# Optimization experiments

Measured on AMD Instinct MI355X. Metric: run time of the kernel, lower is better.

Reference implementation:

```python
import jax, jax.numpy as jnp
import numpy as np

B, A, D, NHEAD, DFF = 8, 128, 256, 8, 2048
EPS = 1e-5


def _ln(x, g, b):
    m = x.mean(-1, keepdims=True)
    v = ((x - m) ** 2).mean(-1, keepdims=True)
    return (x - m) * jax.lax.rsqrt(v + EPS) * g + b


def setup_inputs() -> dict:
    key = jax.random.key(0)
    ks = jax.random.split(key, 32)

    def lin_w(k, i, o):
        s = 1.0 / np.sqrt(i)
        return jax.random.uniform(k, (i, o), jnp.float32, -s, s)

    def lin_b(k, i, o):
        s = 1.0 / np.sqrt(i)
        return jax.random.uniform(k, (o,), jnp.float32, -s, s)

    inp = {
        "src": jax.random.normal(ks[0], (B, A, D), jnp.float32),
        "self_pos_embed": jax.random.normal(ks[1], (B, A, D), jnp.float32),
        "relative_pose_embed": jax.random.normal(ks[2], (B, A, A, D), jnp.float32),
        # q/k/v content projections (D -> D)
        "Wq": lin_w(ks[3], D, D), "bq": lin_b(ks[4], D, D),
        "Wk": lin_w(ks[5], D, D), "bk": lin_b(ks[6], D, D),
        "Wv": lin_w(ks[7], D, D), "bv": lin_b(ks[8], D, D),
        # positional projections (D -> D)
        "Wqp": lin_w(ks[9], D, D), "bqp": lin_b(ks[10], D, D),
        "Wkp": lin_w(ks[11], D, D), "bkp": lin_b(ks[12], D, D),
        "Wvp": lin_w(ks[13], D, D), "bvp": lin_b(ks[14], D, D),
        # FFN
        "W1": lin_w(ks[15], D, DFF), "b1": lin_b(ks[16], D, DFF),
        "W2": lin_w(ks[17], DFF, D), "b2": lin_b(ks[18], DFF, D),
        # LayerNorms
        "g1": jnp.ones((D,), jnp.float32), "be1": jnp.zeros((D,), jnp.float32),
        "g2": jnp.ones((D,), jnp.float32), "be2": jnp.zeros((D,), jnp.float32),
    }
    return inp


def reference(src, self_pos_embed, relative_pose_embed,
              Wq, bq, Wk, bk, Wv, bv, Wqp, bqp, Wkp, bkp, Wvp, bvp,
              W1, b1, W2, b2, g1, be1, g2, be2):
    b_, a_, d_ = src.shape
    H = NHEAD
    hd = (2 * d_) // H          # head dim of concat(q, q_pos) embedding
    H2 = H // 2                  # heads covering the content half / pos half
    vhd = d_ // H                # value head dim (vdim = d_model)
    scale = 1.0 / np.sqrt(hd)

    # Projections. Note: v = sa_v_proj(sa_k_proj(src)) per the original code.
    q_pos = self_pos_embed @ Wqp + bqp                    # (B,A,D)
    k_pos = relative_pose_embed @ Wkp + bkp               # (B,A,A,D)
    v_pos = relative_pose_embed @ Wvp + bvp               # (B,A,A,D)
    k_base = src @ Wk + bk                                # (B,A,D) (broadcast over q instead of repeat)
    v_base = k_base @ Wv + bv                             # (B,A,D)
    q = src @ Wq + bq                                     # (B,A,D)

    # concat([q, q_pos]) / concat([k, k_pos]) split into per-head pieces:
    # first H2 heads come from the content half, last H2 from the pos half.
    qc = q.reshape(b_, a_, H2, hd)
    qp = q_pos.reshape(b_, a_, H2, hd)
    kc = k_base.reshape(b_, a_, H2, hd)
    kp = k_pos.reshape(b_, a_, a_, H2, hd)

    sc = jnp.einsum('bqhe,bkhe->bhqk', qc, kc)            # content heads (k broadcast over q)
    sp = jnp.einsum('bqhe,bqkhe->bhqk', qp, kp)           # relative-pos heads
    scores = jnp.concatenate([sc, sp], axis=1) * scale    # (B,H,A,A)
    attn = jax.nn.softmax(scores, axis=-1)

    vb = v_base.reshape(b_, a_, H, vhd)
    vp = (v_pos).reshape(b_, a_, a_, H, vhd)
    out = jnp.einsum('bhqk,bkhe->bqhe', attn, vb) + \
          jnp.einsum('bhqk,bqkhe->bqhe', attn, vp)        # (B,A,H,vhd)
    src2 = out.reshape(b_, a_, d_)

    x = _ln(src + src2, g1, be1)
    ff = jax.nn.relu(x @ W1 + b1) @ W2 + b2
    return _ln(x + ff, g2, be2)
```

## Files before the change

kernel.cpp:

```cpp
#include <hip/hip_runtime.h>
#include <hip/hip_bf16.h>
#include <math.h>

#define kB 8
#define kA 128
#define kD 256
#define kF 2048
#define NROW 1024

typedef __attribute__((ext_vector_type(8))) __bf16 bf16x8;
typedef __attribute__((ext_vector_type(4))) __bf16 bf16x4;
typedef __attribute__((ext_vector_type(4))) float f32x4;

#define MFMA16(a, b, c) __builtin_amdgcn_mfma_f32_16x16x32_bf16(a, b, c, 0, 0, 0)

__device__ __forceinline__ bf16x8 frag_f32(const float* p) {
    float4 a = *(const float4*)p;
    float4 b = *(const float4*)(p + 4);
    bf16x8 v;
    v[0] = (__bf16)a.x; v[1] = (__bf16)a.y; v[2] = (__bf16)a.z; v[3] = (__bf16)a.w;
    v[4] = (__bf16)b.x; v[5] = (__bf16)b.y; v[6] = (__bf16)b.z; v[7] = (__bf16)b.w;
    return v;
}
__device__ __forceinline__ bf16x8 frag_bf16(const __bf16* p) {
    return *(const bf16x8*)p;
}

__global__ __launch_bounds__(256) void prep_transpose_kernel(
    const float* __restrict__ Wq, const float* __restrict__ Wk,
    const float* __restrict__ Wqp, const float* __restrict__ Wv,
    const float* __restrict__ Wvp, const float* __restrict__ W1,
    const float* __restrict__ W2,
    __bf16* WqT, __bf16* WkT, __bf16* WqpT, __bf16* WvT, __bf16* WvpT,
    __bf16* W1T, __bf16* W2T)
{
    int bid = blockIdx.x;
    const float* in; __bf16* out; int R, C;
    if (bid < 80) {
        int m = bid >> 4; bid &= 15;
        const float* ins[5] = {Wq, Wk, Wqp, Wv, Wvp};
        __bf16* outs[5] = {WqT, WkT, WqpT, WvT, WvpT};
        in = ins[m]; out = outs[m]; R = 256; C = 256;
    } else if (bid < 208) { bid -= 80; in = W1; out = W1T; R = 256; C = 2048; }
    else { bid -= 208; in = W2; out = W2T; R = 2048; C = 256; }
    int tilesC = C >> 6;
    int r0 = (bid / tilesC) << 6, c0 = (bid % tilesC) << 6;
    __shared__ float tile[64][65];
    int t = threadIdx.x, tr = t >> 6, tc = t & 63;
#pragma unroll
    for (int i = 0; i < 16; ++i)
        tile[tr + i * 4][tc] = in[(size_t)(r0 + tr + i * 4) * C + c0 + tc];
    __syncthreads();
#pragma unroll
    for (int i = 0; i < 16; ++i) {
        int oc = tr + i * 4;
        out[(size_t)(c0 + oc) * R + r0 + tc] = (__bf16)tile[tc][oc];
    }
}

__global__ __launch_bounds__(256) void proj3_mfma(
    const float* __restrict__ src, const float* __restrict__ spe,
    const __bf16* __restrict__ WqT, const __bf16* __restrict__ WkT,
    const __bf16* __restrict__ WqpT,
    const float* __restrict__ bq, const float* __restrict__ bk,
    const float* __restrict__ bqp,
    float* __restrict__ q, float* __restrict__ kb, float* __restrict__ qpos)
{
    const float* X; const __bf16* WT; const float* bias; float* Y;
    if (blockIdx.z == 0)      { X = src; WT = WqT;  bias = bq;  Y = q; }
    else if (blockIdx.z == 1) { X = src; WT = WkT;  bias = bk;  Y = kb; }
    else                      { X = spe; WT = WqpT; bias = bqp; Y = qpos; }
    int t = threadIdx.x, w = t >> 6, l = t & 63;
    int p = l & 15, g = l >> 4;
    int m0 = blockIdx.x * 64 + w * 16;
    int n0 = blockIdx.y * 64;
    f32x4 acc[4] = {{0.f,0.f,0.f,0.f},{0.f,0.f,0.f,0.f},{0.f,0.f,0.f,0.f},{0.f,0.f,0.f,0.f}};
#pragma unroll
    for (int ks = 0; ks < 8; ++ks) {
        bf16x8 a = frag_f32(X + (size_t)(m0 + p) * 256 + ks * 32 + g * 8);
#pragma unroll
        for (int nt = 0; nt < 4; ++nt) {
            bf16x8 bb = frag_bf16(WT + (size_t)(n0 + nt * 16 + p) * 256 + ks * 32 + g * 8);
            acc[nt] = MFMA16(a, bb, acc[nt]);
        }
    }
#pragma unroll
    for (int nt = 0; nt < 4; ++nt) {
        int col = n0 + nt * 16 + p;
        float bv = bias[col];
#pragma unroll
        for (int i = 0; i < 4; ++i)
            Y[(size_t)(m0 + g * 4 + i) * 256 + col] = acc[nt][i] + bv;
    }
}

__global__ __launch_bounds__(256) void projv_mfma(
    const float* __restrict__ kb, const __bf16* __restrict__ WvT,
    const float* __restrict__ bv, __bf16* __restrict__ vbT)
{
    int t = threadIdx.x, w = t >> 6, l = t & 63;
    int p = l & 15, g = l >> 4;
    int m0 = blockIdx.x * 64 + w * 16;
    int n0 = blockIdx.y * 64;
    f32x4 acc[4] = {{0.f,0.f,0.f,0.f},{0.f,0.f,0.f,0.f},{0.f,0.f,0.f,0.f},{0.f,0.f,0.f,0.f}};
#pragma unroll
    for (int ks = 0; ks < 8; ++ks) {
        bf16x8 a = frag_f32(kb + (size_t)(m0 + p) * 256 + ks * 32 + g * 8);
#pragma unroll
        for (int nt = 0; nt < 4; ++nt) {
            bf16x8 bb = frag_bf16(WvT + (size_t)(n0 + nt * 16 + p) * 256 + ks * 32 + g * 8);
            acc[nt] = MFMA16(a, bb, acc[nt]);
        }
    }
#pragma unroll
    for (int nt = 0; nt < 4; ++nt) {
        int e = n0 + nt * 16 + p;
        float bvv = bv[e];
#pragma unroll
        for (int i = 0; i < 4; ++i) {
            int row = m0 + g * 4 + i;
            vbT[((size_t)(row >> 7) * 256 + e) * 128 + (row & 127)] =
                (__bf16)(acc[nt][i] + bvv);
        }
    }
}

__global__ __launch_bounds__(256) void u_mfma(
    const float* __restrict__ qpos, const float* __restrict__ Wkp,
    __bf16* __restrict__ u_buf)
{
    int t = threadIdx.x, w = t >> 6, l = t & 63;
    int p = l & 15, g = l >> 4;
    int m0 = blockIdx.x * 16;
    int h = blockIdx.y;
    f32x4 acc[4] = {{0.f,0.f,0.f,0.f},{0.f,0.f,0.f,0.f},{0.f,0.f,0.f,0.f},{0.f,0.f,0.f,0.f}};
#pragma unroll
    for (int ks = 0; ks < 2; ++ks) {
        bf16x8 a = frag_f32(qpos + (size_t)(m0 + p) * 256 + h * 64 + ks * 32 + g * 8);
#pragma unroll
        for (int nt = 0; nt < 4; ++nt) {
            int c0 = w * 64 + nt * 16;
            bf16x8 bb = frag_f32(Wkp + (size_t)(c0 + p) * 256 + h * 64 + ks * 32 + g * 8);
            acc[nt] = MFMA16(a, bb, acc[nt]);
        }
    }
#pragma unroll
    for (int nt = 0; nt < 4; ++nt) {
        int c = w * 64 + nt * 16 + p;
#pragma unroll
        for (int i = 0; i < 4; ++i)
            u_buf[((size_t)(m0 + g * 4 + i) * 4 + h) * 256 + c] = (__bf16)acc[nt][i];
    }
}

__global__ __launch_bounds__(256) void con_mfma(
    const float* __restrict__ q, const float* __restrict__ kb,
    float* __restrict__ s_con)
{
    int t = threadIdx.x, w = t >> 6, l = t & 63;
    int p = l & 15, g = l >> 4;
    int b = blockIdx.x, h = blockIdx.y;
    f32x4 acc[2][8];
#pragma unroll
    for (int mm = 0; mm < 2; ++mm)
#pragma unroll
        for (int nt = 0; nt < 8; ++nt) acc[mm][nt] = (f32x4){0.f,0.f,0.f,0.f};
#pragma unroll
    for (int ks = 0; ks < 2; ++ks) {
        bf16x8 a0 = frag_f32(q + (size_t)(b * 128 + w * 32 + p) * 256 + h * 64 + ks * 32 + g * 8);
        bf16x8 a1 = frag_f32(q + (size_t)(b * 128 + w * 32 + 16 + p) * 256 + h * 64 + ks * 32 + g * 8);
#pragma unroll
        for (int nt = 0; nt < 8; ++nt) {
            bf16x8 bb = frag_f32(kb + (size_t)(b * 128 + nt * 16 + p) * 256 + h * 64 + ks * 32 + g * 8);
            acc[0][nt] = MFMA16(a0, bb, acc[0][nt]);
            acc[1][nt] = MFMA16(a1, bb, acc[1][nt]);
        }
    }
    float* out = s_con + (size_t)(b * 4 + h) * 16384;
#pragma unroll
    for (int mm = 0; mm < 2; ++mm)
#pragma unroll
        for (int nt = 0; nt < 8; ++nt)
#pragma unroll
            for (int i = 0; i < 4; ++i)
                out[(size_t)(w * 32 + mm * 16 + g * 4 + i) * 128 + nt * 16 + p] = acc[mm][nt][i];
}

__global__ __launch_bounds__(256, 2) void attn_mfma(
    const float* __restrict__ src, const float* __restrict__ rel,
    const __bf16* __restrict__ u_buf, const float* __restrict__ s_con,
    const __bf16* __restrict__ vbT, const __bf16* __restrict__ WvpT,
    const float* __restrict__ qpos, const float* __restrict__ bkp,
    const float* __restrict__ bvp, const float* __restrict__ g1,
    const float* __restrict__ be1, float* __restrict__ x_out)
{
    const int t = threadIdx.x, w = t >> 6, l = t & 63;
    const int p = l & 15, g = l >> 4;
    const int qi = blockIdx.x, b = blockIdx.y;
    const int row = b * 128 + qi;

    __shared__ __bf16 Gt[256 * 128];
    __shared__ __bf16 A_lds[16 * 136];
    __shared__ float s_lds[128][9];
    __shared__ float out_lds[256];
    __shared__ float beta_lds[4];
    __shared__ float redA[4], redB[4];

    {
        float v = qpos[(size_t)row * 256 + w * 64 + l] * bkp[w * 64 + l];
#pragma unroll
        for (int sh = 32; sh; sh >>= 1) v += __shfl_xor(v, sh, 64);
        if (l == 0) beta_lds[w] = v;
    }

    {
        f32x4 sacc[2] = {{0.f,0.f,0.f,0.f},{0.f,0.f,0.f,0.f}};
        f32x4 gacc[2][16];
#pragma unroll
        for (int mt = 0; mt < 2; ++mt)
#pragma unroll
            for (int nt = 0; nt < 16; ++nt) gacc[mt][nt] = (f32x4){0.f,0.f,0.f,0.f};
        const float* Rbase = rel + (size_t)row * 128 * 256;
        for (int cs = 0; cs < 8; ++cs) {
            int c0 = cs * 32;
            bf16x8 ua = frag_bf16(u_buf + ((size_t)row * 4 + (p & 3)) * 256 + c0 + g * 8);
            bf16x8 r0 = frag_f32(Rbase + (size_t)(w * 32 + p) * 256 + c0 + g * 8);
            bf16x8 r1 = frag_f32(Rbase + (size_t)(w * 32 + 16 + p) * 256 + c0 + g * 8);
            sacc[0] = MFMA16(ua, r0, sacc[0]);
            sacc[1] = MFMA16(ua, r1, sacc[1]);
#pragma unroll
            for (int nt = 0; nt < 16; ++nt) {
                bf16x8 wv = frag_bf16(WvpT + (size_t)(nt * 16 + p) * 256 + c0 + g * 8);
                gacc[0][nt] = MFMA16(r0, wv, gacc[0][nt]);
                gacc[1][nt] = MFMA16(r1, wv, gacc[1][nt]);
            }
        }
        if (g == 0) {
#pragma unroll
            for (int mt = 0; mt < 2; ++mt)
#pragma unroll
                for (int i = 0; i < 4; ++i)
                    s_lds[w * 32 + mt * 16 + p][4 + i] = sacc[mt][i];
        }
#pragma unroll
        for (int mt = 0; mt < 2; ++mt) {
            int kbase = w * 32 + mt * 16 + g * 4;
            int kb8 = kbase >> 3, klo = kbase & 7;
#pragma unroll
            for (int nt = 0; nt < 16; ++nt) {
                int e = nt * 16 + p;
                bf16x4 v;
                v[0] = (__bf16)gacc[mt][nt][0]; v[1] = (__bf16)gacc[mt][nt][1];
                v[2] = (__bf16)gacc[mt][nt][2]; v[3] = (__bf16)gacc[mt][nt][3];
                *(bf16x4*)&Gt[e * 128 + ((kb8 ^ (e & 7)) << 3) + klo] = v;
            }
        }
    }
    {
        const float* sc = s_con + (size_t)(b * 4) * 16384 + qi * 128;
#pragma unroll
        for (int i = 0; i < 2; ++i) {
            int idx = t + i * 256;
            int h = idx >> 7, k = idx & 127;
            s_lds[k][h] = sc[(size_t)h * 16384 + k];
        }
    }
    __syncthreads();

    {
        int h = t >> 5, l32 = t & 31;
        float beta = (h >= 4) ? beta_lds[h - 4] : 0.f;
        float v0 = (s_lds[l32][h] + beta) * 0.125f;
        float v1 = (s_lds[l32 + 32][h] + beta) * 0.125f;
        float v2 = (s_lds[l32 + 64][h] + beta) * 0.125f;
        float v3 = (s_lds[l32 + 96][h] + beta) * 0.125f;
        float m = fmaxf(fmaxf(v0, v1), fmaxf(v2, v3));
#pragma unroll
        for (int sh = 16; sh; sh >>= 1) m = fmaxf(m, __shfl_xor(m, sh, 64));
        v0 = __expf(v0 - m); v1 = __expf(v1 - m);
        v2 = __expf(v2 - m); v3 = __expf(v3 - m);
        float s = v0 + v1 + v2 + v3;
#pragma unroll
        for (int sh = 16; sh; sh >>= 1) s += __shfl_xor(s, sh, 64);
        float inv = 1.0f / s;
        A_lds[h * 136 + l32]      = (__bf16)(v0 * inv);
        A_lds[h * 136 + l32 + 32] = (__bf16)(v1 * inv);
        A_lds[h * 136 + l32 + 64] = (__bf16)(v2 * inv);
        A_lds[h * 136 + l32 + 96] = (__bf16)(v3 * inv);
    }
    __syncthreads();

    {
        f32x4 oacc[4] = {{0.f,0.f,0.f,0.f},{0.f,0.f,0.f,0.f},{0.f,0.f,0.f,0.f},{0.f,0.f,0.f,0.f}};
        const __bf16* vbase = vbT + (size_t)b * 256 * 128;
#pragma unroll
        for (int ks = 0; ks < 4; ++ks) {
            bf16x8 af = frag_bf16(A_lds + p * 136 + ks * 32 + g * 8);
#pragma unroll
            for (int nt = 0; nt < 4; ++nt) {
                int e = w * 64 + nt * 16 + p;
                bf16x8 vf = frag_bf16(vbase + (size_t)e * 128 + ks * 32 + g * 8);
                oacc[nt] = MFMA16(af, vf, oacc[nt]);
                bf16x8 gf = frag_bf16(&Gt[e * 128 + (((ks * 4 + g) ^ (e & 7)) << 3)]);
                oacc[nt] = MFMA16(af, gf, oacc[nt]);
            }
        }
#pragma unroll
        for (int nt = 0; nt < 4; ++nt) {
            int h = w * 2 + (nt >> 1);
            if (g == (h >> 2)) {
                int i = h & 3;
                float v = (i == 0) ? oacc[nt][0] : (i == 1) ? oacc[nt][1]
                        : (i == 2) ? oacc[nt][2] : oacc[nt][3];
                out_lds[w * 64 + nt * 16 + p] = v;
            }
        }
    }
    __syncthreads();

    {
        float y = src[(size_t)row * 256 + t] + out_lds[t] + bvp[t];
        float s1 = y, s2 = y * y;
#pragma unroll
        for (int sh = 32; sh; sh >>= 1) {
            s1 += __shfl_xor(s1, sh, 64);
            s2 += __shfl_xor(s2, sh, 64);
        }
        if (l == 0) { redA[w] = s1; redB[w] = s2; }
        __syncthreads();
        s1 = redA[0] + redA[1] + redA[2] + redA[3];
        s2 = redB[0] + redB[1] + redB[2] + redB[3];
        float mean = s1 * (1.0f / 256.0f);
        float var = fmaxf(s2 * (1.0f / 256.0f) - mean * mean, 0.0f);
        float inv = rsqrtf(var + 1e-5f);
        x_out[(size_t)row * 256 + t] = (y - mean) * inv * g1[t] + be1[t];
    }
}

__global__ __launch_bounds__(256) void ffn_mfma(
    const float* __restrict__ x, const __bf16* __restrict__ W1T,
    const float* __restrict__ b1, const __bf16* __restrict__ W2T,
    float* __restrict__ part)
{
    __shared__ __bf16 h_lds[32 * 264];
    int t = threadIdx.x, w = t >> 6, l = t & 63;
    int p = l & 15, g = l >> 4;
    int m0 = blockIdx.x * 32;
    int c0 = blockIdx.y * 256;
    int mt = w & 1, nh = w >> 1;

    {
        f32x4 acc[8];
#pragma unroll
        for (int nt = 0; nt < 8; ++nt) acc[nt] = (f32x4){0.f,0.f,0.f,0.f};
#pragma unroll
        for (int ks = 0; ks < 8; ++ks) {
            bf16x8 a = frag_f32(x + (size_t)(m0 + mt * 16 + p) * 256 + ks * 32 + g * 8);
#pragma unroll
            for (int nt = 0; nt < 8; ++nt) {
                bf16x8 bb = frag_bf16(W1T + (size_t)(c0 + nh * 128 + nt * 16 + p) * 256 + ks * 32 + g * 8);
                acc[nt] = MFMA16(a, bb, acc[nt]);
            }
        }
#pragma unroll
        for (int nt = 0; nt < 8; ++nt) {
            int col = nh * 128 + nt * 16 + p;
            float bv = b1[c0 + col];
#pragma unroll
            for (int i = 0; i < 4; ++i)
                h_lds[(mt * 16 + g * 4 + i) * 264 + col] =
                    (__bf16)fmaxf(acc[nt][i] + bv, 0.f);
        }
    }
    __syncthreads();
    {
        f32x4 acc[8];
#pragma unroll
        for (int nt = 0; nt < 8; ++nt) acc[nt] = (f32x4){0.f,0.f,0.f,0.f};
#pragma unroll
        for (int ks = 0; ks < 8; ++ks) {
            bf16x8 a = frag_bf16(h_lds + (mt * 16 + p) * 264 + ks * 32 + g * 8);
#pragma unroll
            for (int nt = 0; nt < 8; ++nt) {
                bf16x8 bb = frag_bf16(W2T + (size_t)(nh * 128 + nt * 16 + p) * 2048 + c0 + ks * 32 + g * 8);
                acc[nt] = MFMA16(a, bb, acc[nt]);
            }
        }
#pragma unroll
        for (int nt = 0; nt < 8; ++nt) {
            int e = nh * 128 + nt * 16 + p;
#pragma unroll
            for (int i = 0; i < 4; ++i)
                part[((size_t)blockIdx.y * NROW + m0 + mt * 16 + g * 4 + i) * 256 + e] = acc[nt][i];
        }
    }
}

__global__ __launch_bounds__(256) void ffn_ln2_kernel(
    const float* __restrict__ x, const float* __restrict__ part,
    const float* __restrict__ b2, const float* __restrict__ g2,
    const float* __restrict__ be2, float* __restrict__ out)
{
    __shared__ float red1[4][4], red2[4][4];
    const int t = threadIdx.x;
    const int r0 = blockIdx.x * 4;
    const int wv = t >> 6, lane = t & 63;
    float b2v = b2[t];
    float yv[4];
#pragma unroll
    for (int r = 0; r < 4; ++r) {
        size_t idx = (size_t)(r0 + r) * 256 + t;
        float y = x[idx] + b2v;
#pragma unroll
        for (int c = 0; c < 8; ++c) y += part[idx + (size_t)c * (NROW * 256)];
        yv[r] = y;
        float s1 = y, s2 = y * y;
#pragma unroll
        for (int sh = 32; sh; sh >>= 1) {
            s1 += __shfl_xor(s1, sh, 64);
            s2 += __shfl_xor(s2, sh, 64);
        }
        if (lane == 0) { red1[r][wv] = s1; red2[r][wv] = s2; }
    }
    __syncthreads();
    float g = g2[t], be = be2[t];
#pragma unroll
    for (int r = 0; r < 4; ++r) {
        float s1 = red1[r][0] + red1[r][1] + red1[r][2] + red1[r][3];
        float s2 = red2[r][0] + red2[r][1] + red2[r][2] + red2[r][3];
        float mean = s1 * (1.0f / 256.0f);
        float var = fmaxf(s2 * (1.0f / 256.0f) - mean * mean, 0.0f);
        float inv = rsqrtf(var + 1e-5f);
        out[(size_t)(r0 + r) * 256 + t] = (yv[r] - mean) * inv * g + be;
    }
}

extern "C" void kernel_launch(void* const* d_in, const int* in_sizes, int n_in,
                              void* d_out, int out_size, void* d_ws, size_t ws_size,
                              hipStream_t stream)
{
    const float* src  = (const float*)d_in[0];
    const float* spe  = (const float*)d_in[1];
    const float* rel  = (const float*)d_in[2];
    const float* Wq   = (const float*)d_in[3];
    const float* bq   = (const float*)d_in[4];
    const float* Wk   = (const float*)d_in[5];
    const float* bk   = (const float*)d_in[6];
    const float* Wv   = (const float*)d_in[7];
    const float* bv   = (const float*)d_in[8];
    const float* Wqp  = (const float*)d_in[9];
    const float* bqp  = (const float*)d_in[10];
    const float* Wkp  = (const float*)d_in[11];
    const float* bkp  = (const float*)d_in[12];
    const float* Wvp  = (const float*)d_in[13];
    const float* bvp  = (const float*)d_in[14];
    const float* W1   = (const float*)d_in[15];
    const float* b1   = (const float*)d_in[16];
    const float* W2   = (const float*)d_in[17];
    const float* b2   = (const float*)d_in[18];
    const float* g1   = (const float*)d_in[19];
    const float* be1  = (const float*)d_in[20];
    const float* g2   = (const float*)d_in[21];
    const float* be2  = (const float*)d_in[22];

    char* wsb = (char*)d_ws;
    const size_t MB = 1 << 20;
    float*  xbuf  = (float*)(wsb);
    float*  q     = (float*)(wsb + 1 * MB);
    float*  kbuf  = (float*)(wsb + 2 * MB);
    float*  qpos  = (float*)(wsb + 3 * MB);
    __bf16* u_buf = (__bf16*)(wsb + 4 * MB);
    float*  s_con = (float*)(wsb + 6 * MB);
    __bf16* vbT   = (__bf16*)(wsb + 8 * MB);
    __bf16* WqT   = (__bf16*)(wsb + 8 * MB + 512 * 1024);
    __bf16* WkT   = WqT + 65536;
    __bf16* WqpT  = WkT + 65536;
    __bf16* WvT   = WqpT + 65536;
    __bf16* WvpT  = WvT + 65536;
    __bf16* W1T   = (__bf16*)(wsb + 9 * MB + 128 * 1024);
    __bf16* W2T   = (__bf16*)(wsb + 10 * MB + 128 * 1024);
    float*  part  = (float*)(wsb + 1 * MB);

    prep_transpose_kernel<<<336, 256, 0, stream>>>(Wq, Wk, Wqp, Wv, Wvp, W1, W2,
                                                   WqT, WkT, WqpT, WvT, WvpT, W1T, W2T);
    proj3_mfma<<<dim3(16, 4, 3), 256, 0, stream>>>(src, spe, WqT, WkT, WqpT,
                                                   bq, bk, bqp, q, kbuf, qpos);
    projv_mfma<<<dim3(16, 4), 256, 0, stream>>>(kbuf, WvT, bv, vbT);
    u_mfma<<<dim3(64, 4), 256, 0, stream>>>(qpos, Wkp, u_buf);
    con_mfma<<<dim3(8, 4), 256, 0, stream>>>(q, kbuf, s_con);
    attn_mfma<<<dim3(kA, kB), 256, 0, stream>>>(src, rel, u_buf, s_con, vbT, WvpT,
                                                qpos, bkp, bvp, g1, be1, xbuf);
    ffn_mfma<<<dim3(32, 8), 256, 0, stream>>>(xbuf, W1T, b1, W2T, part);
    ffn_ln2_kernel<<<256, 256, 0, stream>>>(xbuf, part, b2, g2, be2, (float*)d_out);
}
```

Before: 351.9 us.

## Reassociate relative-pos attention: apply attention to rel rows first, then project with Wvp

```diff
diff --git a/kernel.cpp b/kernel.cpp
--- a/kernel.cpp
+++ b/kernel.cpp
@@ -9,7 +9,6 @@
 #define NROW 1024
 
 typedef __attribute__((ext_vector_type(8))) __bf16 bf16x8;
-typedef __attribute__((ext_vector_type(4))) __bf16 bf16x4;
 typedef __attribute__((ext_vector_type(4))) float f32x4;
 
 #define MFMA16(a, b, c) __builtin_amdgcn_mfma_f32_16x16x32_bf16(a, b, c, 0, 0, 0)
@@ -26,23 +25,22 @@
     return *(const bf16x8*)p;
 }
 
-__global__ __launch_bounds__(256) void prep_transpose_kernel(
+__global__ __launch_bounds__(256) void prep1_kernel(
     const float* __restrict__ Wq, const float* __restrict__ Wk,
-    const float* __restrict__ Wqp, const float* __restrict__ Wv,
-    const float* __restrict__ Wvp, const float* __restrict__ W1,
-    const float* __restrict__ W2,
-    __bf16* WqT, __bf16* WkT, __bf16* WqpT, __bf16* WvT, __bf16* WvpT,
+    const float* __restrict__ Wv, const float* __restrict__ Wvp,
+    const float* __restrict__ W1, const float* __restrict__ W2,
+    __bf16* WqT, __bf16* WkT, __bf16* WvT, __bf16* WvpT,
     __bf16* W1T, __bf16* W2T)
 {
     int bid = blockIdx.x;
     const float* in; __bf16* out; int R, C;
-    if (bid < 80) {
+    if (bid < 64) {
         int m = bid >> 4; bid &= 15;
-        const float* ins[5] = {Wq, Wk, Wqp, Wv, Wvp};
-        __bf16* outs[5] = {WqT, WkT, WqpT, WvT, WvpT};
+        const float* ins[4] = {Wq, Wk, Wv, Wvp};
+        __bf16* outs[4] = {WqT, WkT, WvT, WvpT};
         in = ins[m]; out = outs[m]; R = 256; C = 256;
-    } else if (bid < 208) { bid -= 80; in = W1; out = W1T; R = 256; C = 2048; }
-    else { bid -= 208; in = W2; out = W2T; R = 2048; C = 256; }
+    } else if (bid < 192) { bid -= 64; in = W1; out = W1T; R = 256; C = 2048; }
+    else { bid -= 192; in = W2; out = W2T; R = 2048; C = 256; }
     int tilesC = C >> 6;
     int r0 = (bid / tilesC) << 6, c0 = (bid % tilesC) << 6;
     __shared__ float tile[64][65];
@@ -58,26 +56,64 @@
     }
 }
 
-__global__ __launch_bounds__(256) void proj3_mfma(
-    const float* __restrict__ src, const float* __restrict__ spe,
+__global__ __launch_bounds__(256) void prep2_kernel(
+    const float* __restrict__ Wqp, const float* __restrict__ Wkp,
+    const float* __restrict__ bqp, __bf16* __restrict__ M_hT,
+    float* __restrict__ ubias)
+{
+    int bid = blockIdx.x;
+    int t = threadIdx.x;
+    if (bid < 16) {
+        int h = bid >> 2, cb = bid & 3;
+        int w = t >> 6, l = t & 63, p = l & 15, g = l >> 4;
+        int m0 = cb * 64 + w * 16;
+        f32x4 acc[16];
+#pragma unroll
+        for (int nt = 0; nt < 16; ++nt) acc[nt] = (f32x4){0.f, 0.f, 0.f, 0.f};
+#pragma unroll
+        for (int ks = 0; ks < 2; ++ks) {
+            bf16x8 a = frag_f32(Wkp + (size_t)(m0 + p) * 256 + h * 64 + ks * 32 + g * 8);
+#pragma unroll
+            for (int nt = 0; nt < 16; ++nt) {
+                bf16x8 bb = frag_f32(Wqp + (size_t)(nt * 16 + p) * 256 + h * 64 + ks * 32 + g * 8);
+                acc[nt] = MFMA16(a, bb, acc[nt]);
+            }
+        }
+#pragma unroll
+        for (int nt = 0; nt < 16; ++nt)
+#pragma unroll
+            for (int i = 0; i < 4; ++i)
+                M_hT[((size_t)h * 256 + m0 + g * 4 + i) * 256 + nt * 16 + p] = (__bf16)acc[nt][i];
+    } else {
+        int c = t;
+#pragma unroll
+        for (int h = 0; h < 4; ++h) {
+            float s = 0.f;
+            for (int e = 0; e < 64; ++e) s += bqp[h * 64 + e] * Wkp[(size_t)c * 256 + h * 64 + e];
+            ubias[h * 256 + c] = s;
+        }
+    }
+}
+
+__global__ __launch_bounds__(256) void proj_kernel(
+    const float* __restrict__ src,
     const __bf16* __restrict__ WqT, const __bf16* __restrict__ WkT,
-    const __bf16* __restrict__ WqpT,
     const float* __restrict__ bq, const float* __restrict__ bk,
-    const float* __restrict__ bqp,
-    float* __restrict__ q, float* __restrict__ kb, float* __restrict__ qpos)
-{
-    const float* X; const __bf16* WT; const float* bias; float* Y;
-    if (blockIdx.z == 0)      { X = src; WT = WqT;  bias = bq;  Y = q; }
-    else if (blockIdx.z == 1) { X = src; WT = WkT;  bias = bk;  Y = kb; }
-    else                      { X = spe; WT = WqpT; bias = bqp; Y = qpos; }
+    float* __restrict__ q, float* __restrict__ kb)
+{
+    const __bf16* WT; const float* bias; float* Y;
+    if (blockIdx.z == 0) { WT = WqT; bias = bq; Y = q; }
+    else                 { WT = WkT; bias = bk; Y = kb; }
     int t = threadIdx.x, w = t >> 6, l = t & 63;
     int p = l & 15, g = l >> 4;
     int m0 = blockIdx.x * 64 + w * 16;
     int n0 = blockIdx.y * 64;
-    f32x4 acc[4] = {{0.f,0.f,0.f,0.f},{0.f,0.f,0.f,0.f},{0.f,0.f,0.f,0.f},{0.f,0.f,0.f,0.f}};
+    f32x4 acc[4];
+#pragma unroll
+    for (int nt = 0; nt < 4; ++nt) acc[nt] = (f32x4){0.f, 0.f, 0.f, 0.f};
 #pragma unroll
     for (int ks = 0; ks < 8; ++ks) {
-        bf16x8 a = frag_f32(X + (size_t)(m0 + p) * 256 + ks * 32 + g * 8);
+        bf16x8 a = frag_f32(src + (size_t)(m0 + p) * 256 + ks * 32 + g * 8);
 #pragma unroll
         for (int nt = 0; nt < 4; ++nt) {
             bf16x8 bb = frag_bf16(WT + (size_t)(n0 + nt * 16 + p) * 256 + ks * 32 + g * 8);
@@ -94,7 +130,7 @@
     }
 }
 
-__global__ __launch_bounds__(256) void projv_mfma(
+__global__ __launch_bounds__(256) void projv_kernel(
     const float* __restrict__ kb, const __bf16* __restrict__ WvT,
     const float* __restrict__ bv, __bf16* __restrict__ vbT)
 {
@@ -102,7 +138,9 @@
     int p = l & 15, g = l >> 4;
     int m0 = blockIdx.x * 64 + w * 16;
     int n0 = blockIdx.y * 64;
-    f32x4 acc[4] = {{0.f,0.f,0.f,0.f},{0.f,0.f,0.f,0.f},{0.f,0.f,0.f,0.f},{0.f,0.f,0.f,0.f}};
+    f32x4 acc[4];
+#pragma unroll
+    for (int nt = 0; nt < 4; ++nt) acc[nt] = (f32x4){0.f, 0.f, 0.f, 0.f};
 #pragma unroll
     for (int ks = 0; ks < 8; ++ks) {
         bf16x8 a = frag_f32(kb + (size_t)(m0 + p) * 256 + ks * 32 + g * 8);
@@ -119,280 +157,259 @@
 #pragma unroll
         for (int i = 0; i < 4; ++i) {
             int row = m0 + g * 4 + i;
-            vbT[((size_t)(row >> 7) * 256 + e) * 128 + (row & 127)] =
-                (__bf16)(acc[nt][i] + bvv);
-        }
-    }
-}
-
-__global__ __launch_bounds__(256) void u_mfma(
-    const float* __restrict__ qpos, const float* __restrict__ Wkp,
-    __bf16* __restrict__ u_buf)
+            vbT[((size_t)(row >> 7) * 256 + e) * 128 + (row & 127)] = (__bf16)(acc[nt][i] + bvv);
+        }
+    }
+}
+
+__global__ __launch_bounds__(256) void u_kernel(
+    const float* __restrict__ spe, const __bf16* __restrict__ M_hT,
+    const float* __restrict__ ubias, __bf16* __restrict__ u_buf)
 {
     int t = threadIdx.x, w = t >> 6, l = t & 63;
     int p = l & 15, g = l >> 4;
-    int m0 = blockIdx.x * 16;
     int h = blockIdx.y;
-    f32x4 acc[4] = {{0.f,0.f,0.f,0.f},{0.f,0.f,0.f,0.f},{0.f,0.f,0.f,0.f},{0.f,0.f,0.f,0.f}};
-#pragma unroll
-    for (int ks = 0; ks < 2; ++ks) {
-        bf16x8 a = frag_f32(qpos + (size_t)(m0 + p) * 256 + h * 64 + ks * 32 + g * 8);
-#pragma unroll
-        for (int nt = 0; nt < 4; ++nt) {
-            int c0 = w * 64 + nt * 16;
-            bf16x8 bb = frag_f32(Wkp + (size_t)(c0 + p) * 256 + h * 64 + ks * 32 + g * 8);
+    int m0 = blockIdx.x * 64 + w * 16;
+    f32x4 acc[16];
+#pragma unroll
+    for (int nt = 0; nt < 16; ++nt) acc[nt] = (f32x4){0.f, 0.f, 0.f, 0.f};
+#pragma unroll
+    for (int ks = 0; ks < 8; ++ks) {
+        bf16x8 a = frag_f32(spe + (size_t)(m0 + p) * 256 + ks * 32 + g * 8);
+#pragma unroll
+        for (int nt = 0; nt < 16; ++nt) {
+            bf16x8 bb = frag_bf16(M_hT + ((size_t)h * 256 + nt * 16 + p) * 256 + ks * 32 + g * 8);
             acc[nt] = MFMA16(a, bb, acc[nt]);
         }
     }
 #pragma unroll
-    for (int nt = 0; nt < 4; ++nt) {
-        int c = w * 64 + nt * 16 + p;
+    for (int nt = 0; nt < 16; ++nt) {
+        float ub = ubias[h * 256 + nt * 16 + p];
 #pragma unroll
         for (int i = 0; i < 4; ++i)
-            u_buf[((size_t)(m0 + g * 4 + i) * 4 + h) * 256 + c] = (__bf16)acc[nt][i];
-    }
-}
-
-__global__ __launch_bounds__(256) void con_mfma(
-    const float* __restrict__ q, const float* __restrict__ kb,
-    float* __restrict__ s_con)
-{
-    int t = threadIdx.x, w = t >> 6, l = t & 63;
-    int p = l & 15, g = l >> 4;
-    int b = blockIdx.x, h = blockIdx.y;
-    f32x4 acc[2][8];
-#pragma unroll
-    for (int mm = 0; mm < 2; ++mm)
-#pragma unroll
-        for (int nt = 0; nt < 8; ++nt) acc[mm][nt] = (f32x4){0.f,0.f,0.f,0.f};
-#pragma unroll
-    for (int ks = 0; ks < 2; ++ks) {
-        bf16x8 a0 = frag_f32(q + (size_t)(b * 128 + w * 32 + p) * 256 + h * 64 + ks * 32 + g * 8);
-        bf16x8 a1 = frag_f32(q + (size_t)(b * 128 + w * 32 + 16 + p) * 256 + h * 64 + ks * 32 + g * 8);
-#pragma unroll
-        for (int nt = 0; nt < 8; ++nt) {
-            bf16x8 bb = frag_f32(kb + (size_t)(b * 128 + nt * 16 + p) * 256 + h * 64 + ks * 32 + g * 8);
-            acc[0][nt] = MFMA16(a0, bb, acc[0][nt]);
-            acc[1][nt] = MFMA16(a1, bb, acc[1][nt]);
-        }
-    }
-    float* out = s_con + (size_t)(b * 4 + h) * 16384;
-#pragma unroll
-    for (int mm = 0; mm < 2; ++mm)
-#pragma unroll
-        for (int nt = 0; nt < 8; ++nt)
-#pragma unroll
-            for (int i = 0; i < 4; ++i)
-                out[(size_t)(w * 32 + mm * 16 + g * 4 + i) * 128 + nt * 16 + p] = acc[mm][nt][i];
-}
-
-__global__ __launch_bounds__(256, 2) void attn_mfma(
-    const float* __restrict__ src, const float* __restrict__ rel,
-    const __bf16* __restrict__ u_buf, const float* __restrict__ s_con,
-    const __bf16* __restrict__ vbT, const __bf16* __restrict__ WvpT,
-    const float* __restrict__ qpos, const float* __restrict__ bkp,
-    const float* __restrict__ bvp, const float* __restrict__ g1,
-    const float* __restrict__ be1, float* __restrict__ x_out)
+            u_buf[((size_t)(m0 + g * 4 + i) * 4 + h) * 256 + nt * 16 + p] = (__bf16)(acc[nt][i] + ub);
+    }
+}
+
+__global__ __launch_bounds__(512, 4) void attn1_kernel(
+    const float* __restrict__ rel, const float* __restrict__ q,
+    const float* __restrict__ kb, const __bf16* __restrict__ u_buf,
+    __bf16* __restrict__ A_all, __bf16* __restrict__ r_all)
 {
     const int t = threadIdx.x, w = t >> 6, l = t & 63;
     const int p = l & 15, g = l >> 4;
     const int qi = blockIdx.x, b = blockIdx.y;
     const int row = b * 128 + qi;
 
-    __shared__ __bf16 Gt[256 * 128];
+    __shared__ __bf16 RT[32768];
     __shared__ __bf16 A_lds[16 * 136];
     __shared__ float s_lds[128][9];
-    __shared__ float out_lds[256];
-    __shared__ float beta_lds[4];
-    __shared__ float redA[4], redB[4];
+
+    for (int i = t; i < 8 * 136; i += 512) A_lds[8 * 136 + i] = (__bf16)0.f;
 
     {
-        float v = qpos[(size_t)row * 256 + w * 64 + l] * bkp[w * 64 + l];
-#pragma unroll
-        for (int sh = 32; sh; sh >>= 1) v += __shfl_xor(v, sh, 64);
-        if (l == 0) beta_lds[w] = v;
-    }
+        const float* Rbase = rel + (size_t)row * 128 * 256;
+        const int k = w * 16 + p;
+        const int ko = k >> 3, klo = (k & 7) * 2;
+        f32x4 sacc = (f32x4){0.f, 0.f, 0.f, 0.f};
+#pragma unroll
+        for (int cs = 0; cs < 8; ++cs) {
+            int c0 = cs * 32 + g * 8;
+            bf16x8 rf = frag_f32(Rbase + (size_t)k * 256 + c0);
+            bf16x8 ua = frag_bf16(u_buf + ((size_t)row * 4 + (p & 3)) * 256 + c0);
+            sacc = MFMA16(ua, rf, sacc);
+#pragma unroll
+            for (int j = 0; j < 8; ++j) {
+                int byte = (c0 + j) * 256 + ((ko ^ j) << 4) + klo;
+                *(__bf16*)((char*)RT + byte) = rf[j];
+            }
+        }
+        f32x4 cacc[4];
+#pragma unroll
+        for (int h = 0; h < 4; ++h) cacc[h] = (f32x4){0.f, 0.f, 0.f, 0.f};
+#pragma unroll
+        for (int h = 0; h < 4; ++h)
+#pragma unroll
+            for (int ks = 0; ks < 2; ++ks) {
+                bf16x8 qa = frag_f32(q + (size_t)row * 256 + h * 64 + ks * 32 + g * 8);
+                bf16x8 kf = frag_f32(kb + ((size_t)b * 128 + k) * 256 + h * 64 + ks * 32 + g * 8);
+                cacc[h] = MFMA16(qa, kf, cacc[h]);
+            }
+        if (g == 0) {
+#pragma unroll
+            for (int i = 0; i < 4; ++i) s_lds[k][4 + i] = sacc[i];
+#pragma unroll
+            for (int h = 0; h < 4; ++h) s_lds[k][h] = cacc[h][0];
+        }
+    }
+    __syncthreads();
 
     {
-        f32x4 sacc[2] = {{0.f,0.f,0.f,0.f},{0.f,0.f,0.f,0.f}};
-        f32x4 gacc[2][16];
-#pragma unroll
-        for (int mt = 0; mt < 2; ++mt)
-#pragma unroll
-            for (int nt = 0; nt < 16; ++nt) gacc[mt][nt] = (f32x4){0.f,0.f,0.f,0.f};
-        const float* Rbase = rel + (size_t)row * 128 * 256;
+        float v0 = s_lds[l][w] * 0.125f;
+        float v1 = s_lds[l + 64][w] * 0.125f;
+        float m = fmaxf(v0, v1);
+#pragma unroll
+        for (int sh = 32; sh; sh >>= 1) m = fmaxf(m, __shfl_xor(m, sh, 64));
+        v0 = __expf(v0 - m); v1 = __expf(v1 - m);
+        float s = v0 + v1;
+#pragma unroll
+        for (int sh = 32; sh; sh >>= 1) s += __shfl_xor(s, sh, 64);
+        float inv = 1.0f / s;
+        __bf16 e0 = (__bf16)(v0 * inv), e1 = (__bf16)(v1 * inv);
+        A_lds[w * 136 + l] = e0;
+        A_lds[w * 136 + l + 64] = e1;
+        __bf16* Ag = A_all + ((size_t)(b * 8 + w) * 128 + qi) * 128;
+        Ag[l] = e0; Ag[l + 64] = e1;
+    }
+    __syncthreads();
+
+    {
+        f32x4 racc[2];
+        racc[0] = (f32x4){0.f, 0.f, 0.f, 0.f};
+        racc[1] = (f32x4){0.f, 0.f, 0.f, 0.f};
+#pragma unroll
+        for (int ks = 0; ks < 4; ++ks) {
+            bf16x8 af = *(const bf16x8*)&A_lds[p * 136 + ks * 32 + g * 8];
+#pragma unroll
+            for (int nt = 0; nt < 2; ++nt) {
+                int c = w * 32 + nt * 16 + p;
+                bf16x8 bfr = *(const bf16x8*)((char*)RT + c * 256 + (((ks * 4 + g) ^ (c & 7)) << 4));
+                racc[nt] = MFMA16(af, bfr, racc[nt]);
+            }
+        }
+        if (g < 2) {
+#pragma unroll
+            for (int nt = 0; nt < 2; ++nt)
+#pragma unroll
+                for (int i = 0; i < 4; ++i)
+                    r_all[((size_t)row * 8 + g * 4 + i) * 256 + w * 32 + nt * 16 + p] =
+                        (__bf16)racc[nt][i];
+        }
+    }
+}
+
+__global__ __launch_bounds__(256) void attn2_kernel(
+    const float* __restrict__ src, const __bf16* __restrict__ A_all,
+    const __bf16* __restrict__ r_all, const __bf16* __restrict__ vbT,
+    const __bf16* __restrict__ WvpT, const float* __restrict__ bvp,
+    const float* __restrict__ g1, const float* __restrict__ be1,
+    float* __restrict__ x_out)
+{
+    const int t = threadIdx.x, w = t >> 6, l = t & 63;
+    const int p = l & 15, g = l >> 4;
+    const int r0 = blockIdx.x * 4;
+    const int b = r0 >> 7, q0 = r0 & 127;
+    __shared__ float ymem[4][260];
+
+    f32x4 oacc[4];
+#pragma unroll
+    for (int nt = 0; nt < 4; ++nt) oacc[nt] = (f32x4){0.f, 0.f, 0.f, 0.f};
+#pragma unroll
+    for (int nt = 0; nt < 4; ++nt) {
+        int e0 = w * 64 + nt * 16;
+        int h = e0 >> 5;
+#pragma unroll
+        for (int ks = 0; ks < 4; ++ks) {
+            bf16x8 af = frag_bf16(A_all + ((size_t)(b * 8 + h) * 128 + q0 + p) * 128 + ks * 32 + g * 8);
+            bf16x8 vf = frag_bf16(vbT + ((size_t)b * 256 + e0 + p) * 128 + ks * 32 + g * 8);
+            oacc[nt] = MFMA16(af, vf, oacc[nt]);
+        }
+#pragma unroll
         for (int cs = 0; cs < 8; ++cs) {
-            int c0 = cs * 32;
-            bf16x8 ua = frag_bf16(u_buf + ((size_t)row * 4 + (p & 3)) * 256 + c0 + g * 8);
-            bf16x8 r0 = frag_f32(Rbase + (size_t)(w * 32 + p) * 256 + c0 + g * 8);
-            bf16x8 r1 = frag_f32(Rbase + (size_t)(w * 32 + 16 + p) * 256 + c0 + g * 8);
-            sacc[0] = MFMA16(ua, r0, sacc[0]);
-            sacc[1] = MFMA16(ua, r1, sacc[1]);
-#pragma unroll
-            for (int nt = 0; nt < 16; ++nt) {
-                bf16x8 wv = frag_bf16(WvpT + (size_t)(nt * 16 + p) * 256 + c0 + g * 8);
-                gacc[0][nt] = MFMA16(r0, wv, gacc[0][nt]);
-                gacc[1][nt] = MFMA16(r1, wv, gacc[1][nt]);
-            }
-        }
-        if (g == 0) {
-#pragma unroll
-            for (int mt = 0; mt < 2; ++mt)
-#pragma unroll
-                for (int i = 0; i < 4; ++i)
-                    s_lds[w * 32 + mt * 16 + p][4 + i] = sacc[mt][i];
-        }
-#pragma unroll
-        for (int mt = 0; mt < 2; ++mt) {
-            int kbase = w * 32 + mt * 16 + g * 4;
-            int kb8 = kbase >> 3, klo = kbase & 7;
-#pragma unroll
-            for (int nt = 0; nt < 16; ++nt) {
-                int e = nt * 16 + p;
-                bf16x4 v;
-                v[0] = (__bf16)gacc[mt][nt][0]; v[1] = (__bf16)gacc[mt][nt][1];
-                v[2] = (__bf16)gacc[mt][nt][2]; v[3] = (__bf16)gacc[mt][nt][3];
-                *(bf16x4*)&Gt[e * 128 + ((kb8 ^ (e & 7)) << 3) + klo] = v;
-            }
-        }
-    }
+            bf16x8 rf = frag_bf16(r_all + ((size_t)(r0 + p) * 8 + h) * 256 + cs * 32 + g * 8);
+            bf16x8 wf = frag_bf16(WvpT + (size_t)(e0 + p) * 256 + cs * 32 + g * 8);
+            oacc[nt] = MFMA16(rf, wf, oacc[nt]);
+        }
+    }
+    if (g == 0) {
+#pragma unroll
+        for (int nt = 0; nt < 4; ++nt)
+#pragma unroll
+            for (int i = 0; i < 4; ++i)
+                ymem[i][w * 64 + nt * 16 + p] = oacc[nt][i];
+    }
+    __syncthreads();
+
     {
-        const float* sc = s_con + (size_t)(b * 4) * 16384 + qi * 128;
-#pragma unroll
-        for (int i = 0; i < 2; ++i) {
-            int idx = t + i * 256;
-            int h = idx >> 7, k = idx & 127;
-            s_lds[k][h] = sc[(size_t)h * 16384 + k];
-        }
-    }
-    __syncthreads();
-
-    {
-        int h = t >> 5, l32 = t & 31;
-        float beta = (h >= 4) ? beta_lds[h - 4] : 0.f;
-        float v0 = (s_lds[l32][h] + beta) * 0.125f;
-        float v1 = (s_lds[l32 + 32][h] + beta) * 0.125f;
-        float v2 = (s_lds[l32 + 64][h] + beta) * 0.125f;
-        float v3 = (s_lds[l32 + 96][h] + beta) * 0.125f;
-        float m = fmaxf(fmaxf(v0, v1), fmaxf(v2, v3));
-#pragma unroll
-        for (int sh = 16; sh; sh >>= 1) m = fmaxf(m, __shfl_xor(m, sh, 64));
-        v0 = __expf(v0 - m); v1 = __expf(v1 - m);
-        v2 = __expf(v2 - m); v3 = __expf(v3 - m);
-        float s = v0 + v1 + v2 + v3;
-#pragma unroll
-        for (int sh = 16; sh; sh >>= 1) s += __shfl_xor(s, sh, 64);
-        float inv = 1.0f / s;
-        A_lds[h * 136 + l32]      = (__bf16)(v0 * inv);
-        A_lds[h * 136 + l32 + 32] = (__bf16)(v1 * inv);
-        A_lds[h * 136 + l32 + 64] = (__bf16)(v2 * inv);
-        A_lds[h * 136 + l32 + 96] = (__bf16)(v3 * inv);
-    }
-    __syncthreads();
-
-    {
-        f32x4 oacc[4] = {{0.f,0.f,0.f,0.f},{0.f,0.f,0.f,0.f},{0.f,0.f,0.f,0.f},{0.f,0.f,0.f,0.f}};
-        const __bf16* vbase = vbT + (size_t)b * 256 * 128;
-#pragma unroll
-        for (int ks = 0; ks < 4; ++ks) {
-            bf16x8 af = frag_bf16(A_lds + p * 136 + ks * 32 + g * 8);
-#pragma unroll
-            for (int nt = 0; nt < 4; ++nt) {
-                int e = w * 64 + nt * 16 + p;
-                bf16x8 vf = frag_bf16(vbase + (size_t)e * 128 + ks * 32 + g * 8);
-                oacc[nt] = MFMA16(af, vf, oacc[nt]);
-                bf16x8 gf = frag_bf16(&Gt[e * 128 + (((ks * 4 + g) ^ (e & 7)) << 3)]);
-                oacc[nt] = MFMA16(af, gf, oacc[nt]);
-            }
-        }
-#pragma unroll
-        for (int nt = 0; nt < 4; ++nt) {
-            int h = w * 2 + (nt >> 1);
-            if (g == (h >> 2)) {
-                int i = h & 3;
-                float v = (i == 0) ? oacc[nt][0] : (i == 1) ? oacc[nt][1]
-                        : (i == 2) ? oacc[nt][2] : oacc[nt][3];
-                out_lds[w * 64 + nt * 16 + p] = v;
-            }
-        }
-    }
-    __syncthreads();
-
-    {
-        float y = src[(size_t)row * 256 + t] + out_lds[t] + bvp[t];
-        float s1 = y, s2 = y * y;
+        float vals[4];
+        float s1 = 0.f, s2 = 0.f;
+#pragma unroll
+        for (int j = 0; j < 4; ++j) {
+            int e = l + j * 64;
+            float v = src[(size_t)(r0 + w) * 256 + e] + ymem[w][e] + bvp[e];
+            vals[j] = v; s1 += v; s2 += v * v;
+        }
 #pragma unroll
         for (int sh = 32; sh; sh >>= 1) {
             s1 += __shfl_xor(s1, sh, 64);
             s2 += __shfl_xor(s2, sh, 64);
         }
-        if (l == 0) { redA[w] = s1; redB[w] = s2; }
-        __syncthreads();
-        s1 = redA[0] + redA[1] + redA[2] + redA[3];
-        s2 = redB[0] + redB[1] + redB[2] + redB[3];
         float mean = s1 * (1.0f / 256.0f);
         float var = fmaxf(s2 * (1.0f / 256.0f) - mean * mean, 0.0f);
         float inv = rsqrtf(var + 1e-5f);
-        x_out[(size_t)row * 256 + t] = (y - mean) * inv * g1[t] + be1[t];
-    }
-}
-
-__global__ __launch_bounds__(256) void ffn_mfma(
+#pragma unroll
+        for (int j = 0; j < 4; ++j) {
+            int e = l + j * 64;
+            x_out[(size_t)(r0 + w) * 256 + e] = (vals[j] - mean) * inv * g1[e] + be1[e];
+        }
+    }
+}
+
+__global__ __launch_bounds__(256) void ffn_kernel(
     const float* __restrict__ x, const __bf16* __restrict__ W1T,
     const float* __restrict__ b1, const __bf16* __restrict__ W2T,
     float* __restrict__ part)
 {
-    __shared__ __bf16 h_lds[32 * 264];
+    __shared__ __bf16 h_lds[16 * 264];
     int t = threadIdx.x, w = t >> 6, l = t & 63;
     int p = l & 15, g = l >> 4;
-    int m0 = blockIdx.x * 32;
+    int m0 = blockIdx.x * 16;
     int c0 = blockIdx.y * 256;
-    int mt = w & 1, nh = w >> 1;
 
     {
-        f32x4 acc[8];
-#pragma unroll
-        for (int nt = 0; nt < 8; ++nt) acc[nt] = (f32x4){0.f,0.f,0.f,0.f};
+        f32x4 acc[4];
+#pragma unroll
+        for (int nt = 0; nt < 4; ++nt) acc[nt] = (f32x4){0.f, 0.f, 0.f, 0.f};
 #pragma unroll
         for (int ks = 0; ks < 8; ++ks) {
-            bf16x8 a = frag_f32(x + (size_t)(m0 + mt * 16 + p) * 256 + ks * 32 + g * 8);
-#pragma unroll
-            for (int nt = 0; nt < 8; ++nt) {
-                bf16x8 bb = frag_bf16(W1T + (size_t)(c0 + nh * 128 + nt * 16 + p) * 256 + ks * 32 + g * 8);
+            bf16x8 a = frag_f32(x + (size_t)(m0 + p) * 256 + ks * 32 + g * 8);
+#pragma unroll
+            for (int nt = 0; nt < 4; ++nt) {
+                int hc = w * 64 + nt * 16 + p;
+                bf16x8 bb = frag_bf16(W1T + (size_t)(c0 + hc) * 256 + ks * 32 + g * 8);
                 acc[nt] = MFMA16(a, bb, acc[nt]);
             }
         }
 #pragma unroll
-        for (int nt = 0; nt < 8; ++nt) {
-            int col = nh * 128 + nt * 16 + p;
-            float bv = b1[c0 + col];
+        for (int nt = 0; nt < 4; ++nt) {
+            int hc = w * 64 + nt * 16 + p;
+            float bv = b1[c0 + hc];
 #pragma unroll
             for (int i = 0; i < 4; ++i)
-                h_lds[(mt * 16 + g * 4 + i) * 264 + col] =
-                    (__bf16)fmaxf(acc[nt][i] + bv, 0.f);
+                h_lds[(g * 4 + i) * 264 + hc] = (__bf16)fmaxf(acc[nt][i] + bv, 0.f);
         }
     }
     __syncthreads();
     {
-        f32x4 acc[8];
-#pragma unroll
-        for (int nt = 0; nt < 8; ++nt) acc[nt] = (f32x4){0.f,0.f,0.f,0.f};
+        f32x4 acc[4];
+#pragma unroll
+        for (int nt = 0; nt < 4; ++nt) acc[nt] = (f32x4){0.f, 0.f, 0.f, 0.f};
 #pragma unroll
         for (int ks = 0; ks < 8; ++ks) {
-            bf16x8 a = frag_bf16(h_lds + (mt * 16 + p) * 264 + ks * 32 + g * 8);
-#pragma unroll
-            for (int nt = 0; nt < 8; ++nt) {
-                bf16x8 bb = frag_bf16(W2T + (size_t)(nh * 128 + nt * 16 + p) * 2048 + c0 + ks * 32 + g * 8);
+            bf16x8 a = *(const bf16x8*)&h_lds[p * 264 + ks * 32 + g * 8];
+#pragma unroll
+            for (int nt = 0; nt < 4; ++nt) {
+                int e = w * 64 + nt * 16 + p;
+                bf16x8 bb = frag_bf16(W2T + (size_t)e * 2048 + c0 + ks * 32 + g * 8);
                 acc[nt] = MFMA16(a, bb, acc[nt]);
             }
         }
 #pragma unroll
-        for (int nt = 0; nt < 8; ++nt) {
-            int e = nh * 128 + nt * 16 + p;
+        for (int nt = 0; nt < 4; ++nt)
 #pragma unroll
             for (int i = 0; i < 4; ++i)
-                part[((size_t)blockIdx.y * NROW + m0 + mt * 16 + g * 4 + i) * 256 + e] = acc[nt][i];
-        }
+                part[((size_t)blockIdx.y * NROW + m0 + g * 4 + i) * 256 + w * 64 + nt * 16 + p] =
+                    acc[nt][i];
     }
 }
 
@@ -462,34 +479,36 @@
     const float* be1  = (const float*)d_in[20];
     const float* g2   = (const float*)d_in[21];
     const float* be2  = (const float*)d_in[22];
+    (void)bkp;
 
     char* wsb = (char*)d_ws;
     const size_t MB = 1 << 20;
     float*  xbuf  = (float*)(wsb);
     float*  q     = (float*)(wsb + 1 * MB);
-    float*  kbuf  = (float*)(wsb + 2 * MB);
-    float*  qpos  = (float*)(wsb + 3 * MB);
-    __bf16* u_buf = (__bf16*)(wsb + 4 * MB);
-    float*  s_con = (float*)(wsb + 6 * MB);
-    __bf16* vbT   = (__bf16*)(wsb + 8 * MB);
-    __bf16* WqT   = (__bf16*)(wsb + 8 * MB + 512 * 1024);
+    float*  kb    = (float*)(wsb + 2 * MB);
+    __bf16* A_all = (__bf16*)(wsb + 3 * MB);
+    __bf16* r_all = (__bf16*)(wsb + 5 * MB);
+    float*  part  = (float*)(wsb + 1 * MB);
+    __bf16* u_buf = (__bf16*)(wsb + 9 * MB);
+    __bf16* vbT   = (__bf16*)(wsb + 11 * MB);
+    __bf16* WqT   = (__bf16*)(wsb + 11 * MB + 512 * 1024);
     __bf16* WkT   = WqT + 65536;
-    __bf16* WqpT  = WkT + 65536;
-    __bf16* WvT   = WqpT + 65536;
+    __bf16* WvT   = WkT + 65536;
     __bf16* WvpT  = WvT + 65536;
-    __bf16* W1T   = (__bf16*)(wsb + 9 * MB + 128 * 1024);
-    __bf16* W2T   = (__bf16*)(wsb + 10 * MB + 128 * 1024);
-    float*  part  = (float*)(wsb + 1 * MB);
-
-    prep_transpose_kernel<<<336, 256, 0, stream>>>(Wq, Wk, Wqp, Wv, Wvp, W1, W2,
-                                                   WqT, WkT, WqpT, WvT, WvpT, W1T, W2T);
-    proj3_mfma<<<dim3(16, 4, 3), 256, 0, stream>>>(src, spe, WqT, WkT, WqpT,
-                                                   bq, bk, bqp, q, kbuf, qpos);
-    projv_mfma<<<dim3(16, 4), 256, 0, stream>>>(kbuf, WvT, bv, vbT);
-    u_mfma<<<dim3(64, 4), 256, 0, stream>>>(qpos, Wkp, u_buf);
-    con_mfma<<<dim3(8, 4), 256, 0, stream>>>(q, kbuf, s_con);
-    attn_mfma<<<dim3(kA, kB), 256, 0, stream>>>(src, rel, u_buf, s_con, vbT, WvpT,
-                                                qpos, bkp, bvp, g1, be1, xbuf);
-    ffn_mfma<<<dim3(32, 8), 256, 0, stream>>>(xbuf, W1T, b1, W2T, part);
+    __bf16* W1T   = (__bf16*)(wsb + 12 * MB);
+    __bf16* W2T   = (__bf16*)(wsb + 13 * MB);
+    __bf16* M_hT  = (__bf16*)(wsb + 14 * MB);
+    float*  ubias = (float*)(wsb + 14 * MB + 512 * 1024);
+
+    prep1_kernel<<<320, 256, 0, stream>>>(Wq, Wk, Wv, Wvp, W1, W2,
+                                          WqT, WkT, WvT, WvpT, W1T, W2T);
+    prep2_kernel<<<17, 256, 0, stream>>>(Wqp, Wkp, bqp, M_hT, ubias);
+    proj_kernel<<<dim3(16, 4, 2), 256, 0, stream>>>(src, WqT, WkT, bq, bk, q, kb);
+    projv_kernel<<<dim3(16, 4), 256, 0, stream>>>(kb, WvT, bv, vbT);
+    u_kernel<<<dim3(16, 4), 256, 0, stream>>>(spe, M_hT, ubias, u_buf);
+    attn1_kernel<<<dim3(kA, kB), 512, 0, stream>>>(rel, q, kb, u_buf, A_all, r_all);
+    attn2_kernel<<<256, 256, 0, stream>>>(src, A_all, r_all, vbT, WvpT, bvp,
+                                          g1, be1, xbuf);
+    ffn_kernel<<<dim3(64, 8), 256, 0, stream>>>(xbuf, W1T, b1, W2T, part);
     ffn_ln2_kernel<<<256, 256, 0, stream>>>(xbuf, part, b2, g2, be2, (float*)d_out);
 }
```

Result: no change. 349.7 us (-0.7%).
